# Kernel tuning notes

Measured on AMD Instinct MI355X. Metric: run time of the kernel, lower is better.

## Reference

```python
import jax, jax.numpy as jnp
import numpy as np

# dims: S spaces, B batch, T tokens, D = dense_dim = concept_dim, K codebook size
S, B, T, D, K = 8, 8, 2048, 64, 512
BN_EPS = 1e-3  # keras BatchNormalization default


def setup_inputs() -> dict:
    key = jax.random.key(0)
    k0, k1, k2 = jax.random.split(key, 3)
    x = jax.random.normal(k0, (B, T, D), jnp.float32)
    W = jax.random.normal(k1, (S, D, D), jnp.float32) * 0.1   # per-space Dense kernels
    b = jnp.zeros((S, D), jnp.float32)                         # per-space Dense biases
    gamma = jnp.ones((S, D), jnp.float32)                      # BN scale
    beta = jnp.zeros((S, D), jnp.float32)                      # BN shift
    bn_mean = jnp.zeros((S, D), jnp.float32)                   # BN moving mean
    bn_var = jnp.ones((S, D), jnp.float32)                     # BN moving var
    E = jax.random.normal(k2, (S, K, D), jnp.float32)          # per-space codebooks
    return dict(x=x, W=W, b=b, gamma=gamma, beta=beta,
                bn_mean=bn_mean, bn_var=bn_var, E=E)


def reference(x, W, b, gamma, beta, bn_mean, bn_var, E):
    # per-space projection: Dense -> BatchNorm (inference) -> softmax gate
    proj = jnp.einsum('btd,sde->sbte', x, W) + b[:, None, None, :]          # [S,B,T,D]
    inv = jax.lax.rsqrt(bn_var + BN_EPS)
    bn = gamma[:, None, None, :] * (proj - bn_mean[:, None, None, :]) * inv[:, None, None, :] \
         + beta[:, None, None, :]
    att = jax.nn.softmax(bn, axis=-1)
    z = x[None] * att                                                       # z_e_att, [S,B,T,D]

    # squared euclidean distance to each code; argmin(norm) == argmin(dist^2)
    d2 = (jnp.sum(z * z, axis=-1, keepdims=True)
          - 2.0 * jnp.einsum('sbtc,skc->sbtk', z, E)
          + jnp.sum(E * E, axis=-1)[:, None, None, :])                      # [S,B,T,K]
    z_k = jnp.argmin(d2, axis=-1)                                           # [S,B,T] int

    # gather nearest codes per space, then add_n over spaces (set_att != 0)
    z_q_s = E[jnp.arange(S)[:, None, None], z_k]                            # [S,B,T,D]
    z_q = jnp.sum(z_q_s, axis=0)                                            # [B,T,D]
    z_e = jnp.sum(z, axis=0)                                                # [B,T,D]
    z_k = z_k.astype(jnp.int64) if z_k.dtype != jnp.int64 else z_k          # tf.argmin -> int64
    return z_q, z_e, z_k
```

## Files before the change

### kernel.cpp

```cpp
#include <hip/hip_runtime.h>
#include <cfloat>
#include <cmath>

#define SN 8
#define DN 64
#define KN 512
#define NN 16384
#define CK 64
#define REPAIR_THR 2e-3f
#define GAP_IK 4u
#define MAXFLAG 32768

#define WS_CNT 0
#define WS_SCL 16
#define WS_OFF (16 + SN*DN)
#define WS_E2  (WS_OFF + SN*DN)
#define WS_ENT (WS_E2 + SN*KN)
#define WS_WTH (WS_ENT + MAXFLAG)
#define WS_WTL (WS_WTH + SN*64*32)
#define WS_EH  (WS_WTL + SN*64*32)
#define WS_EL  (WS_EH + SN*KN*32)
#define WS_ZP  (WS_EL + SN*KN*32)
#define WS_E2S (WS_ZP + SN*NN*DN)
#define WS_END (WS_E2S + SN*KN)

#define LDS_ZH 0
#define LDS_ZL 16384
#define LDS_E0 32768
#define LDS_TOTAL 65536

#define FB_LDS_R2    17408
#define FB_LDS_TAIL  33792
#define FB_LDS_TOTAL 34816

typedef __attribute__((ext_vector_type(8))) short bf16x8;
typedef __attribute__((ext_vector_type(4))) short s16x4;
typedef __attribute__((ext_vector_type(4))) float f32x4;

__device__ inline short bf_hi(float f, float& rem) {
    unsigned u = __float_as_uint(f);
    unsigned r = (u + 0x7fffu + ((u >> 16) & 1u)) & 0xffff0000u;
    rem = f - __uint_as_float(r);
    return (short)(r >> 16);
}
__device__ inline short bf_rn(float f) {
    unsigned u = __float_as_uint(f);
    return (short)((u + 0x7fffu + ((u >> 16) & 1u)) >> 16);
}
__device__ inline void cvt4(float a, float b, float c, float d, s16x4& h, s16x4& l) {
    float r0, r1, r2, r3;
    h.x = bf_hi(a, r0); h.y = bf_hi(b, r1); h.z = bf_hi(c, r2); h.w = bf_hi(d, r3);
    l.x = bf_rn(r0); l.y = bf_rn(r1); l.z = bf_rn(r2); l.w = bf_rn(r3);
}
__device__ inline float bf2f(unsigned short h) {
    return __uint_as_float(((unsigned)h) << 16);
}

union U8 { bf16x8 v; s16x4 q[2]; };

__global__ void prep_all_kernel(const float* __restrict__ b, const float* __restrict__ gamma,
                                const float* __restrict__ beta, const float* __restrict__ bmean,
                                const float* __restrict__ bvar, const float* __restrict__ W,
                                const float* __restrict__ E, float* __restrict__ ws) {
    __shared__ float wt[64][65];
    const int blk = blockIdx.x, tid = threadIdx.x;
    if (blk < 256) {
        int idx = blk * 256 + tid;
        int sk = idx >> 4, c4 = idx & 15;
        int k = sk & (KN - 1);
        float4 g = ((const float4*)E)[(size_t)sk * 16 + c4];
        s16x4 h4, l4;
        cvt4(g.x, g.y, g.z, g.w, h4, l4);
        size_t off = ((size_t)sk * 128 + c4 * 8) ^ ((k & 7) << 4);
        *(s16x4*)((char*)(ws + WS_EH) + off) = h4;
        *(s16x4*)((char*)(ws + WS_EL) + off) = l4;
    } else if (blk < 264) {
        int s = blk - 256;
        #pragma unroll
        for (int r = 0; r < 4; ++r) {
            int i = r * 256 + tid;
            float4 g = ((const float4*)W)[(size_t)s * 1024 + i];
            int d = i >> 4, c4 = i & 15;
            wt[d][c4 * 4 + 0] = g.x; wt[d][c4 * 4 + 1] = g.y;
            wt[d][c4 * 4 + 2] = g.z; wt[d][c4 * 4 + 3] = g.w;
        }
        __syncthreads();
        #pragma unroll
        for (int r = 0; r < 4; ++r) {
            int j = r * 256 + tid;
            int e = j >> 4, c4 = j & 15;
            s16x4 h4, l4;
            cvt4(wt[c4 * 4 + 0][e], wt[c4 * 4 + 1][e], wt[c4 * 4 + 2][e], wt[c4 * 4 + 3][e], h4, l4);
            size_t off = (size_t)(s * 64 + e) * 128 + c4 * 8;
            *(s16x4*)((char*)(ws + WS_WTH) + off) = h4;
            *(s16x4*)((char*)(ws + WS_WTL) + off) = l4;
        }
    } else {
        if (blk == 264 && tid < 16) ((int*)ws)[tid] = 0;
        int t2 = (blk - 264) * 256 + tid;
        if (t2 < SN * KN) {
            const float* er = E + (size_t)t2 * DN;
            double a = 0.0;
            for (int d = 0; d < DN; ++d) { double v = (double)er[d]; a = fma(v, v, a); }
            ws[WS_E2 + t2]  = (float)a;
            ws[WS_E2S + t2] = (float)(a * 4096.0);
        }
        int u = t2 - SN * KN;
        if (u >= 0 && u < SN * DN) {
            double inv = 1.0 / sqrt((double)bvar[u] + 0.001);
            double sc  = (double)gamma[u] * inv;
            ws[WS_SCL + u] = (float)sc;
            ws[WS_OFF + u] = (float)(((double)b[u] - (double)bmean[u]) * sc + (double)beta[u]);
        }
    }
}

__global__ void prep_kernel(const float* __restrict__ b, const float* __restrict__ gamma,
                            const float* __restrict__ beta, const float* __restrict__ bmean,
                            const float* __restrict__ bvar, const float* __restrict__ E,
                            float* __restrict__ ws) {
    int tid = blockIdx.x * 256 + threadIdx.x;
    if (tid < SN * KN) {
        const float* er = E + (size_t)tid * DN;
        double a = 0.0;
        for (int d = 0; d < DN; ++d) { double v = (double)er[d]; a = fma(v, v, a); }
        ws[WS_E2 + tid] = (float)a;
    }
    int u = tid - SN * KN;
    if (u >= 0 && u < SN * DN) {
        double inv = 1.0 / sqrt((double)bvar[u] + 0.001);
        double sc  = (double)gamma[u] * inv;
        ws[WS_SCL + u] = (float)sc;
        ws[WS_OFF + u] = (float)(((double)b[u] - (double)bmean[u]) * sc + (double)beta[u]);
    }
}

__launch_bounds__(512, 4)
__global__ void main_kernel(const float* __restrict__ x, float* __restrict__ ws,
                            float* __restrict__ out, int entcap) {
    extern __shared__ char smraw[];
    const int tid = threadIdx.x;
    const int s  = blockIdx.y;
    const int n0 = blockIdx.x * 128;
    const int lane = tid & 63;
    const int w    = tid >> 6;
    const int cc   = lane & 15;
    const int kq   = lane >> 4;
    const int arow = w * 16 + cc;
    const int axor = (arow & 7) << 4;

    const char* eimg_h = (const char*)(ws + WS_EH) + (size_t)s * KN * 128;
    const char* eimg_l = (const char*)(ws + WS_EL) + (size_t)s * KN * 128;

    float4 pf0 = *(const float4*)(eimg_h + tid * 16);
    float4 pf1 = *(const float4*)(eimg_l + tid * 16);

    U8 xah[2], xal[2];
    #pragma unroll
    for (int ks = 0; ks < 2; ++ks) {
        const float* xr = x + (size_t)(n0 + arow) * DN + ks * 32 + kq * 8;
        float4 a = *(const float4*)xr;
        float4 b2 = *(const float4*)(xr + 4);
        s16x4 h0, l0, h1, l1;
        cvt4(a.x, a.y, a.z, a.w, h0, l0);
        cvt4(b2.x, b2.y, b2.z, b2.w, h1, l1);
        xah[ks].q[0] = h0; xah[ks].q[1] = h1;
        xal[ks].q[0] = l0; xal[ks].q[1] = l1;
    }

    const char* wimg_h = (const char*)(ws + WS_WTH) + (size_t)s * 64 * 128;
    const char* wimg_l = (const char*)(ws + WS_WTL) + (size_t)s * 64 * 128;
    f32x4 pa[4];
    #pragma unroll
    for (int nt = 0; nt < 4; ++nt) pa[nt] = (f32x4){0.f, 0.f, 0.f, 0.f};
    #pragma unroll
    for (int ks = 0; ks < 2; ++ks) {
        #pragma unroll
        for (int nt = 0; nt < 4; ++nt) {
            int brow = nt * 16 + cc;
            bf16x8 bh = *(const bf16x8*)(wimg_h + brow * 128 + ks * 64 + kq * 16);
            bf16x8 bl = *(const bf16x8*)(wimg_l + brow * 128 + ks * 64 + kq * 16);
            pa[nt] = __builtin_amdgcn_mfma_f32_16x16x32_bf16(xah[ks].v, bh, pa[nt], 0, 0, 0);
            pa[nt] = __builtin_amdgcn_mfma_f32_16x16x32_bf16(xah[ks].v, bl, pa[nt], 0, 0, 0);
            pa[nt] = __builtin_amdgcn_mfma_f32_16x16x32_bf16(xal[ks].v, bh, pa[nt], 0, 0, 0);
        }
    }

    float sclv[4], oflv[4];
    #pragma unroll
    for (int nt = 0; nt < 4; ++nt) {
        sclv[nt] = ws[WS_SCL + s * 64 + nt * 16 + cc];
        oflv[nt] = ws[WS_OFF + s * 64 + nt * 16 + cc];
    }
    float zzq[4];
    #pragma unroll
    for (int r = 0; r < 4; ++r) {
        int t = w * 16 + kq * 4 + r;
        float v0 = fmaf(pa[0][r], sclv[0], oflv[0]);
        float v1 = fmaf(pa[1][r], sclv[1], oflv[1]);
        float v2 = fmaf(pa[2][r], sclv[2], oflv[2]);
        float v3 = fmaf(pa[3][r], sclv[3], oflv[3]);
        float mx = fmaxf(fmaxf(v0, v1), fmaxf(v2, v3));
        mx = fmaxf(mx, __shfl_xor(mx, 1)); mx = fmaxf(mx, __shfl_xor(mx, 2));
        mx = fmaxf(mx, __shfl_xor(mx, 4)); mx = fmaxf(mx, __shfl_xor(mx, 8));
        float e0 = __expf(v0 - mx), e1 = __expf(v1 - mx);
        float e2v = __expf(v2 - mx), e3 = __expf(v3 - mx);
        float sm = e0 + e1 + e2v + e3;
        sm += __shfl_xor(sm, 1); sm += __shfl_xor(sm, 2);
        sm += __shfl_xor(sm, 4); sm += __shfl_xor(sm, 8);
        float inv = 1.0f / sm;
        float att[4] = { e0 * inv, e1 * inv, e2v * inv, e3 * inv };
        float zz = 0.f;
        int txor = (t & 7) << 4;
        #pragma unroll
        for (int nt = 0; nt < 4; ++nt) {
            int e = nt * 16 + cc;
            float xv = x[(size_t)(n0 + t) * DN + e];
            float z = xv * att[nt];
            zz += z * z;
            float rem; short zh = bf_hi(z, rem); short zl = bf_rn(rem);
            int zoff = (t * 128 + e * 2) ^ txor;
            *(short*)(smraw + LDS_ZH + zoff) = zh;
            *(short*)(smraw + LDS_ZL + zoff) = zl;
        }
        zz += __shfl_xor(zz, 1); zz += __shfl_xor(zz, 2);
        zz += __shfl_xor(zz, 4); zz += __shfl_xor(zz, 8);
        zzq[r] = (zz + 16.f) * 4096.f;
    }

    bf16x8 zah[2], zal[2];
    #pragma unroll
    for (int ks = 0; ks < 2; ++ks) {
        int aoff = (arow * 128 + kq * 16 + ks * 64) ^ axor;
        zah[ks] = *(const bf16x8*)(smraw + LDS_ZH + aoff);
        zal[ks] = *(const bf16x8*)(smraw + LDS_ZL + aoff);
    }

    {
        char* eb = smraw + LDS_E0;
        *(float4*)(eb + tid * 16) = pf0;
        *(float4*)(eb + 8192 + tid * 16) = pf1;
    }
    __syncthreads();

    #pragma unroll
    for (int j = 0; j < 4; ++j) {
        int a = tid + j * 512;
        int t = a >> 4, q = a & 15;
        int off = (t * 128 + q * 8) ^ ((t & 7) << 4);
        s16x4 h = *(const s16x4*)(smraw + LDS_ZH + off);
        s16x4 l = *(const s16x4*)(smraw + LDS_ZL + off);
        float4 zv;
        zv.x = bf2f((unsigned short)h.x) + bf2f((unsigned short)l.x);
        zv.y = bf2f((unsigned short)h.y) + bf2f((unsigned short)l.y);
        zv.z = bf2f((unsigned short)h.z) + bf2f((unsigned short)l.z);
        zv.w = bf2f((unsigned short)h.w) + bf2f((unsigned short)l.w);
        ((float4*)(ws + WS_ZP))[((size_t)s * NN + n0 + t) * 16 + q] = zv;
    }

    unsigned m1[4], m2[4];
    #pragma unroll
    for (int r = 0; r < 4; ++r) { m1[r] = 0xFFFFFFFFu; m2[r] = 0xFFFFFFFFu; }

    int p = 0;
    #pragma unroll 1
    for (int c = 0; c < KN / CK; ++c) {
        const char* ebuf = smraw + LDS_E0 + p * 16384;
        int kk = c * CK;
        if (c < KN / CK - 1) {
            pf0 = *(const float4*)(eimg_h + (size_t)(kk + CK) * 128 + tid * 16);
            pf1 = *(const float4*)(eimg_l + (size_t)(kk + CK) * 128 + tid * 16);
        }
        float e2v[4];
        #pragma unroll
        for (int nt = 0; nt < 4; ++nt) e2v[nt] = ws[WS_E2S + s * KN + kk + nt * 16 + cc];

        f32x4 acc[4];
        #pragma unroll
        for (int nt = 0; nt < 4; ++nt) acc[nt] = (f32x4){0.f, 0.f, 0.f, 0.f};
        #pragma unroll
        for (int ks = 0; ks < 2; ++ks) {
            #pragma unroll
            for (int nt = 0; nt < 4; ++nt) {
                int brow = nt * 16 + cc;
                int boff = (brow * 128 + kq * 16 + ks * 64) ^ ((brow & 7) << 4);
                bf16x8 bh = *(const bf16x8*)(ebuf + boff);
                bf16x8 bl = *(const bf16x8*)(ebuf + 8192 + boff);
                acc[nt] = __builtin_amdgcn_mfma_f32_16x16x32_bf16(zah[ks], bh, acc[nt], 0, 0, 0);
                acc[nt] = __builtin_amdgcn_mfma_f32_16x16x32_bf16(zah[ks], bl, acc[nt], 0, 0, 0);
                acc[nt] = __builtin_amdgcn_mfma_f32_16x16x32_bf16(zal[ks], bh, acc[nt], 0, 0, 0);
            }
        }
        #pragma unroll
        for (int nt = 0; nt < 4; ++nt) {
            unsigned kx = (unsigned)(kk + nt * 16 + cc);
            #pragma unroll
            for (int r = 0; r < 4; ++r) {
                float cell = fmaf(-8192.f, acc[nt][r], zzq[r] + e2v[nt]);
                unsigned key = (((unsigned)cell) << 9) | kx;
                m2[r] = min(m2[r], max(m1[r], key));
                m1[r] = min(m1[r], key);
            }
        }
        if (c < KN / CK - 1) {
            char* nb = smraw + LDS_E0 + (p ^ 1) * 16384;
            *(float4*)(nb + tid * 16) = pf0;
            *(float4*)(nb + 8192 + tid * 16) = pf1;
            __syncthreads();
            p ^= 1;
        }
    }

    #pragma unroll
    for (int mask = 1; mask <= 8; mask <<= 1) {
        #pragma unroll
        for (int r = 0; r < 4; ++r) {
            unsigned o1 = (unsigned)__shfl_xor((int)m1[r], mask);
            unsigned o2 = (unsigned)__shfl_xor((int)m2[r], mask);
            unsigned hi = max(m1[r], o1);
            m1[r] = min(m1[r], o1);
            m2[r] = min(min(m2[r], o2), hi);
        }
    }
    #pragma unroll
    for (int r = 0; r < 4; ++r) {
        int n = n0 + w * 16 + kq * 4 + r;
        if (cc == 0) {
            int k1 = (int)(m1[r] & 511u);
            out[2 * NN * DN + s * NN + n] = (float)k1;
            if ((m2[r] >> 9) - (m1[r] >> 9) <= GAP_IK) {
                int idx = atomicAdd((int*)ws, 1);
                if (idx < entcap) ((int*)ws)[WS_ENT + idx] = (s << 14) | n;
            }
        }
    }
}

__launch_bounds__(256, 4)
__global__ void main_fb_kernel(const float* __restrict__ x, const float* __restrict__ W,
                               const float* __restrict__ E, float* __restrict__ ws,
                               float* __restrict__ out, int entcap) {
    extern __shared__ char smraw[];
    float4* xs4 = (float4*)smraw;
    float4* ws4 = (float4*)(smraw + FB_LDS_R2);
    char* ehb = smraw;
    char* elb = smraw + 8192;
    char* zhb = smraw + FB_LDS_R2;
    char* zlb = smraw + FB_LDS_R2 + 8192;
    float* tailf = (float*)(smraw + FB_LDS_TAIL);
    float* e2s = tailf; float* scl = tailf + 64; float* ofl = tailf + 128; float* zzs = tailf + 192;

    const int tid = threadIdx.x;
    const int tg = tid >> 4, lg = tid & 15;
    const int s  = blockIdx.y;
    const int n0 = blockIdx.x * 64;
    const float4* xg4 = (const float4*)x;
    const float4* Wg4 = (const float4*)W;
    const float4* Eg4 = (const float4*)E;

    #pragma unroll
    for (int r = 0; r < 4; ++r) {
        int i = r * 256 + tid;
        xs4[(i >> 4) * 17 + (i & 15)] = xg4[n0 * 16 + i];
        ws4[i] = Wg4[s * 1024 + i];
    }
    if (tid < 64) { scl[tid] = ws[WS_SCL + s * 64 + tid]; ofl[tid] = ws[WS_OFF + s * 64 + tid]; }
    __syncthreads();

    float pa[4][4];
    #pragma unroll
    for (int ti = 0; ti < 4; ++ti)
        #pragma unroll
        for (int j = 0; j < 4; ++j) pa[ti][j] = 0.f;
    #pragma unroll 4
    for (int c = 0; c < 16; ++c) {
        float4 xv[4], wv[4];
        #pragma unroll
        for (int ti = 0; ti < 4; ++ti) xv[ti] = xs4[(tg * 4 + ti) * 17 + c];
        #pragma unroll
        for (int dd = 0; dd < 4; ++dd) wv[dd] = ws4[(c * 4 + dd) * 16 + lg];
        #pragma unroll
        for (int ti = 0; ti < 4; ++ti) {
            float a0 = pa[ti][0], a1 = pa[ti][1], a2 = pa[ti][2], a3 = pa[ti][3];
            a0 = fmaf(xv[ti].x, wv[0].x, a0); a0 = fmaf(xv[ti].y, wv[1].x, a0);
            a0 = fmaf(xv[ti].z, wv[2].x, a0); a0 = fmaf(xv[ti].w, wv[3].x, a0);
            a1 = fmaf(xv[ti].x, wv[0].y, a1); a1 = fmaf(xv[ti].y, wv[1].y, a1);
            a1 = fmaf(xv[ti].z, wv[2].y, a1); a1 = fmaf(xv[ti].w, wv[3].y, a1);
            a2 = fmaf(xv[ti].x, wv[0].z, a2); a2 = fmaf(xv[ti].y, wv[1].z, a2);
            a2 = fmaf(xv[ti].z, wv[2].z, a2); a2 = fmaf(xv[ti].w, wv[3].z, a2);
            a3 = fmaf(xv[ti].x, wv[0].w, a3); a3 = fmaf(xv[ti].y, wv[1].w, a3);
            a3 = fmaf(xv[ti].z, wv[2].w, a3); a3 = fmaf(xv[ti].w, wv[3].w, a3);
            pa[ti][0] = a0; pa[ti][1] = a1; pa[ti][2] = a2; pa[ti][3] = a3;
        }
    }
    __syncthreads();

    {
        float s0 = scl[lg * 4 + 0], s1 = scl[lg * 4 + 1], s2 = scl[lg * 4 + 2], s3 = scl[lg * 4 + 3];
        float o0 = ofl[lg * 4 + 0], o1 = ofl[lg * 4 + 1], o2 = ofl[lg * 4 + 2], o3 = ofl[lg * 4 + 3];
        #pragma unroll
        for (int ti = 0; ti < 4; ++ti) {
            int t = tg * 4 + ti;
            float v0 = fmaf(pa[ti][0], s0, o0);
            float v1 = fmaf(pa[ti][1], s1, o1);
            float v2 = fmaf(pa[ti][2], s2, o2);
            float v3 = fmaf(pa[ti][3], s3, o3);
            float mx = fmaxf(fmaxf(v0, v1), fmaxf(v2, v3));
            mx = fmaxf(mx, __shfl_xor(mx, 1)); mx = fmaxf(mx, __shfl_xor(mx, 2));
            mx = fmaxf(mx, __shfl_xor(mx, 4)); mx = fmaxf(mx, __shfl_xor(mx, 8));
            float e0 = expf(v0 - mx), e1 = expf(v1 - mx), e2v = expf(v2 - mx), e3 = expf(v3 - mx);
            float sm = e0 + e1 + e2v + e3;
            sm += __shfl_xor(sm, 1); sm += __shfl_xor(sm, 2);
            sm += __shfl_xor(sm, 4); sm += __shfl_xor(sm, 8);
            float inv = 1.0f / sm;
            float4 xv = xs4[t * 17 + lg];
            float z0 = xv.x * (e0 * inv), z1 = xv.y * (e1 * inv);
            float z2 = xv.z * (e2v * inv), z3 = xv.w * (e3 * inv);
            float zz = z0 * z0 + z1 * z1 + z2 * z2 + z3 * z3;
            zz += __shfl_xor(zz, 1); zz += __shfl_xor(zz, 2);
            zz += __shfl_xor(zz, 4); zz += __shfl_xor(zz, 8);
            if (lg == 0) zzs[t] = zz;
            s16x4 h4, l4;
            cvt4(z0, z1, z2, z3, h4, l4);
            int zoff = (t * 128 + lg * 8) ^ ((t & 7) << 4);
            *(s16x4*)(zhb + zoff) = h4;
            *(s16x4*)(zlb + zoff) = l4;
            float* pz = out + NN * DN + (size_t)(n0 + t) * DN + lg * 4;
            atomicAdd(pz + 0, z0); atomicAdd(pz + 1, z1);
            atomicAdd(pz + 2, z2); atomicAdd(pz + 3, z3);
        }
    }
    __syncthreads();

    const int lane = tid & 63;
    const int w    = tid >> 6;
    const int arow = w * 16 + (lane & 15);
    const int kg16 = (lane >> 4) * 16;
    const int axor = (arow & 7) << 4;
    const int abase = arow * 128 + kg16;

    float zzv[4];
    #pragma unroll
    for (int r = 0; r < 4; ++r) zzv[r] = zzs[w * 16 + (lane >> 4) * 4 + r];

    float m1[4], m2[4]; int k1[4];
    #pragma unroll
    for (int r = 0; r < 4; ++r) { m1[r] = FLT_MAX; m2[r] = FLT_MAX; k1[r] = 0x7fffffff; }

    for (int kk = 0; kk < KN; kk += CK) {
        __syncthreads();
        #pragma unroll
        for (int r = 0; r < 4; ++r) {
            int i = r * 256 + tid;
            float4 g = Eg4[(s * KN + kk) * 16 + i];
            int row = i >> 4, c4 = i & 15;
            s16x4 h4, l4;
            cvt4(g.x, g.y, g.z, g.w, h4, l4);
            int off = (row * 128 + c4 * 8) ^ ((row & 7) << 4);
            *(s16x4*)(ehb + off) = h4;
            *(s16x4*)(elb + off) = l4;
        }
        if (tid < 64) e2s[tid] = ws[WS_E2 + s * KN + kk + tid];
        __syncthreads();

        f32x4 acc[4];
        #pragma unroll
        for (int nt = 0; nt < 4; ++nt) acc[nt] = (f32x4){0.f, 0.f, 0.f, 0.f};
        #pragma unroll
        for (int ks = 0; ks < 2; ++ks) {
            int aoff = (abase + ks * 64) ^ axor;
            bf16x8 ah = *(const bf16x8*)(zhb + aoff);
            bf16x8 al = *(const bf16x8*)(zlb + aoff);
            #pragma unroll
            for (int nt = 0; nt < 4; ++nt) {
                int brow = nt * 16 + (lane & 15);
                int boff = (brow * 128 + kg16 + ks * 64) ^ ((brow & 7) << 4);
                bf16x8 bh = *(const bf16x8*)(ehb + boff);
                bf16x8 bl = *(const bf16x8*)(elb + boff);
                acc[nt] = __builtin_amdgcn_mfma_f32_16x16x32_bf16(ah, bh, acc[nt], 0, 0, 0);
                acc[nt] = __builtin_amdgcn_mfma_f32_16x16x32_bf16(ah, bl, acc[nt], 0, 0, 0);
                acc[nt] = __builtin_amdgcn_mfma_f32_16x16x32_bf16(al, bh, acc[nt], 0, 0, 0);
            }
        }
        #pragma unroll
        for (int nt = 0; nt < 4; ++nt) {
            float e2v = e2s[nt * 16 + (lane & 15)];
            int kx = kk + nt * 16 + (lane & 15);
            #pragma unroll
            for (int r = 0; r < 4; ++r) {
                float d2 = fmaf(-2.0f, acc[nt][r], zzv[r]) + e2v;
                if (d2 < m1[r]) { m2[r] = m1[r]; m1[r] = d2; k1[r] = kx; }
                else if (d2 < m2[r]) { m2[r] = d2; }
            }
        }
    }

    #pragma unroll
    for (int mask = 1; mask <= 8; mask <<= 1) {
        #pragma unroll
        for (int r = 0; r < 4; ++r) {
            float om1 = __shfl_xor(m1[r], mask);
            int   ok1 = __shfl_xor(k1[r], mask);
            float om2 = __shfl_xor(m2[r], mask);
            bool better = (om1 < m1[r]) || (om1 == m1[r] && ok1 < k1[r]);
            float nm2 = better ? fminf(m1[r], om2) : fminf(om1, m2[r]);
            if (better) { m1[r] = om1; k1[r] = ok1; }
            m2[r] = nm2;
        }
    }
    #pragma unroll
    for (int r = 0; r < 4; ++r) {
        int t = w * 16 + (lane >> 4) * 4 + r;
        int n = n0 + t;
        if ((lane & 15) == 0) {
            out[2 * NN * DN + s * NN + n] = (float)k1[r];
            if (m2[r] - m1[r] < REPAIR_THR) {
                int idx = atomicAdd((int*)ws, 1);
                if (idx < entcap) ((int*)ws)[WS_ENT + idx] = (s << 14) | n;
            }
        }
        int kb = __shfl(k1[r], lane & 48);
        float4 eg = Eg4[(s * KN + kb) * 16 + (lane & 15)];
        float* q = out + (size_t)n * DN + (lane & 15) * 4;
        atomicAdd(q + 0, eg.x); atomicAdd(q + 1, eg.y);
        atomicAdd(q + 2, eg.z); atomicAdd(q + 3, eg.w);
    }
}

__global__ void reduce_kernel(const float* __restrict__ E, const float* __restrict__ ws,
                              float* __restrict__ out) {
    int idx = blockIdx.x * 256 + threadIdx.x;
    int n = idx >> 4, c = idx & 15;
    const float4* zp4 = (const float4*)(ws + WS_ZP);
    float4 ze = make_float4(0.f, 0.f, 0.f, 0.f);
    #pragma unroll
    for (int s = 0; s < SN; ++s) {
        float4 v = zp4[((size_t)s * NN + n) * 16 + c];
        ze.x += v.x; ze.y += v.y; ze.z += v.z; ze.w += v.w;
    }
    ((float4*)out)[NN * 16 + (size_t)n * 16 + c] = ze;

    float4 zq = make_float4(0.f, 0.f, 0.f, 0.f);
    #pragma unroll
    for (int s = 0; s < SN; ++s) {
        int k = (int)(out[2 * NN * DN + s * NN + n] + 0.5f);
        float4 e = ((const float4*)E)[((size_t)s * KN + k) * 16 + c];
        zq.x += e.x; zq.y += e.y; zq.z += e.z; zq.w += e.w;
    }
    ((float4*)out)[(size_t)n * 16 + c] = zq;
}

__global__ void repair_kernel(const float* __restrict__ x, const float* __restrict__ W,
                              const float* __restrict__ b, const float* __restrict__ gamma,
                              const float* __restrict__ beta, const float* __restrict__ bmean,
                              const float* __restrict__ bvar, const float* __restrict__ E,
                              float* __restrict__ ws, float* __restrict__ out, int entcap) {
    __shared__ double zd[64];
    __shared__ double red[256];
    __shared__ int redk[256];
    __shared__ double zzsh;
    __shared__ int shk[2];
    int cnt = ((int*)ws)[0]; if (cnt > entcap) cnt = entcap;
    const int tid = threadIdx.x;
    for (int idx = blockIdx.x; idx < cnt; idx += gridDim.x) {
        int code = ((int*)ws)[WS_ENT + idx];
        int s = code >> 14, n = code & (NN - 1);
        int e = tid & 63, q = tid >> 6;
        const float* xrow = x + (size_t)n * 64;
        double p0 = 0.0, p1 = 0.0, p2 = 0.0, p3 = 0.0;
        for (int d = q * 16; d < q * 16 + 16; d += 4) {
            p0 = fma((double)xrow[d],     (double)W[((size_t)s * 64 + d) * 64 + e],     p0);
            p1 = fma((double)xrow[d + 1], (double)W[((size_t)s * 64 + d + 1) * 64 + e], p1);
            p2 = fma((double)xrow[d + 2], (double)W[((size_t)s * 64 + d + 2) * 64 + e], p2);
            p3 = fma((double)xrow[d + 3], (double)W[((size_t)s * 64 + d + 3) * 64 + e], p3);
        }
        red[tid] = (p0 + p1) + (p2 + p3);
        __syncthreads();
        if (tid < 64) {
            double proj = (red[tid] + red[tid + 64]) + (red[tid + 128] + red[tid + 192]);
            double inv = 1.0 / sqrt((double)bvar[s * 64 + e] + 0.001);
            double bn = (double)gamma[s * 64 + e] * ((proj + (double)b[s * 64 + e]) - (double)bmean[s * 64 + e]) * inv
                      + (double)beta[s * 64 + e];
            double m = bn;
            #pragma unroll
            for (int mask = 1; mask <= 32; mask <<= 1) m = fmax(m, __shfl_xor(m, mask));
            double ex = exp(bn - m);
            double sm = ex;
            #pragma unroll
            for (int mask = 1; mask <= 32; mask <<= 1) sm += __shfl_xor(sm, mask);
            double z = (double)xrow[e] * (ex / sm);
            zd[e] = z;
            double zz = z * z;
            #pragma unroll
            for (int mask = 1; mask <= 32; mask <<= 1) zz += __shfl_xor(zz, mask);
            if (tid == 0) zzsh = zz;
        }
        __syncthreads();
        double bv = DBL_MAX; int bk = 1 << 30;
        for (int k = tid; k < KN; k += 256) {
            const float* er = E + ((size_t)s * KN + k) * 64;
            double d0 = 0.0, d1 = 0.0, d2a = 0.0, d3 = 0.0;
            double f0 = 0.0, f1 = 0.0, f2 = 0.0, f3 = 0.0;
            for (int d = 0; d < 64; d += 4) {
                double e0 = (double)er[d], e1 = (double)er[d + 1];
                double e2d = (double)er[d + 2], e3d = (double)er[d + 3];
                d0 = fma(zd[d], e0, d0);     d1 = fma(zd[d + 1], e1, d1);
                d2a = fma(zd[d + 2], e2d, d2a); d3 = fma(zd[d + 3], e3d, d3);
                f0 = fma(e0, e0, f0); f1 = fma(e1, e1, f1);
                f2 = fma(e2d, e2d, f2); f3 = fma(e3d, e3d, f3);
            }
            double dot = (d0 + d1) + (d2a + d3);
            double e2t = (f0 + f1) + (f2 + f3);
            double d2v = (zzsh - 2.0 * dot) + e2t;
            if (d2v < bv) { bv = d2v; bk = k; }
        }
        #pragma unroll
        for (int mask = 1; mask <= 32; mask <<= 1) {
            double ov = __shfl_xor(bv, mask);
            int   ok = __shfl_xor(bk, mask);
            if (ov < bv || (ov == bv && ok < bk)) { bv = ov; bk = ok; }
        }
        if ((tid & 63) == 0) { red[tid >> 6] = bv; redk[tid >> 6] = bk; }
        __syncthreads();
        if (tid == 0) {
            double m = red[0]; int mk = redk[0];
            for (int i = 1; i < 4; ++i)
                if (red[i] < m || (red[i] == m && redk[i] < mk)) { m = red[i]; mk = redk[i]; }
            int kold = (int)(out[2 * NN * 64 + s * NN + n] + 0.5f);
            shk[0] = mk; shk[1] = kold;
            out[2 * NN * 64 + s * NN + n] = (float)mk;
        }
        __syncthreads();
        int mk = shk[0], kold = shk[1];
        if (mk != kold && tid < 64)
            atomicAdd(out + n * 64 + tid, E[((size_t)s * KN + mk) * 64 + tid] - E[((size_t)s * KN + kold) * 64 + tid]);
        __syncthreads();
    }
}

extern "C" void kernel_launch(void* const* d_in, const int* in_sizes, int n_in,
                              void* d_out, int out_size, void* d_ws, size_t ws_size,
                              hipStream_t stream) {
    const float* x     = (const float*)d_in[0];
    const float* W     = (const float*)d_in[1];
    const float* b     = (const float*)d_in[2];
    const float* gamma = (const float*)d_in[3];
    const float* beta  = (const float*)d_in[4];
    const float* bmean = (const float*)d_in[5];
    const float* bvar  = (const float*)d_in[6];
    const float* E     = (const float*)d_in[7];
    float* out = (float*)d_out;
    float* ws  = (float*)d_ws;

    bool staged = ws_size >= (size_t)WS_END * 4;

    long avail = (long)(ws_size / 4) - WS_ENT - 16;
    if (avail < 0) avail = 0;
    int entcap = (int)(avail > MAXFLAG ? MAXFLAG : avail);
    if (staged) entcap = MAXFLAG;

    if (staged) {
        hipFuncSetAttribute((const void*)main_kernel, hipFuncAttributeMaxDynamicSharedMemorySize, LDS_TOTAL);
        prep_all_kernel<<<282, 256, 0, stream>>>(b, gamma, beta, bmean, bvar, W, E, ws);
        dim3 grid(128, 8);
        main_kernel<<<grid, 512, LDS_TOTAL, stream>>>(x, ws, out, entcap);
        reduce_kernel<<<1024, 256, 0, stream>>>(E, ws, out);
    } else {
        hipMemsetAsync(d_ws, 0, 64, stream);
        prep_kernel<<<18, 256, 0, stream>>>(b, gamma, beta, bmean, bvar, E, ws);
        hipMemsetAsync(d_out, 0, (size_t)(2 * NN * DN) * sizeof(float), stream);
        dim3 grid(256, 8);
        main_fb_kernel<<<grid, 256, FB_LDS_TOTAL, stream>>>(x, W, E, ws, out, entcap);
    }
    repair_kernel<<<2048, 256, 0, stream>>>(x, W, b, gamma, beta, bmean, bvar, E, ws, out, entcap);
}
```

Before: 150.3 us.

## Read codebook MFMA operands directly from global memory instead of LDS double buffer

Removes the double-buffered LDS staging of the bf16 hi/lo codebook images in the main distance kernel, so each wave loads B operands straight from global or L2 memory. Only the z tiles stay in shared memory, so the allocation halves and launch bounds are raised to allow more resident blocks. The prep kernel stops writing the XOR-swizzled layout to match. This drops the per-chunk barriers and LDS stores, but every wave now re-reads the same codebook rows from cache with no prefetch, which may expose memory latency.

```diff
diff --git a/kernel.cpp b/kernel.cpp
--- a/kernel.cpp
+++ b/kernel.cpp
@@ -26,8 +26,7 @@
 
 #define LDS_ZH 0
 #define LDS_ZL 16384
-#define LDS_E0 32768
-#define LDS_TOTAL 65536
+#define LDS_TOTAL 32768
 
 #define FB_LDS_R2    17408
 #define FB_LDS_TAIL  33792
@@ -67,11 +66,10 @@
     if (blk < 256) {
         int idx = blk * 256 + tid;
         int sk = idx >> 4, c4 = idx & 15;
-        int k = sk & (KN - 1);
         float4 g = ((const float4*)E)[(size_t)sk * 16 + c4];
         s16x4 h4, l4;
         cvt4(g.x, g.y, g.z, g.w, h4, l4);
-        size_t off = ((size_t)sk * 128 + c4 * 8) ^ ((k & 7) << 4);
+        size_t off = (size_t)sk * 128 + c4 * 8;
         *(s16x4*)((char*)(ws + WS_EH) + off) = h4;
         *(s16x4*)((char*)(ws + WS_EL) + off) = l4;
     } else if (blk < 264) {
@@ -135,7 +133,7 @@
     }
 }
 
-__launch_bounds__(512, 4)
+__launch_bounds__(512, 8)
 __global__ void main_kernel(const float* __restrict__ x, float* __restrict__ ws,
                             float* __restrict__ out, int entcap) {
     extern __shared__ char smraw[];
@@ -151,9 +149,6 @@
 
     const char* eimg_h = (const char*)(ws + WS_EH) + (size_t)s * KN * 128;
     const char* eimg_l = (const char*)(ws + WS_EL) + (size_t)s * KN * 128;
-
-    float4 pf0 = *(const float4*)(eimg_h + tid * 16);
-    float4 pf1 = *(const float4*)(eimg_l + tid * 16);
 
     U8 xah[2], xal[2];
     #pragma unroll
@@ -235,12 +230,6 @@
         zah[ks] = *(const bf16x8*)(smraw + LDS_ZH + aoff);
         zal[ks] = *(const bf16x8*)(smraw + LDS_ZL + aoff);
     }
-
-    {
-        char* eb = smraw + LDS_E0;
-        *(float4*)(eb + tid * 16) = pf0;
-        *(float4*)(eb + 8192 + tid * 16) = pf1;
-    }
     __syncthreads();
 
     #pragma unroll
@@ -262,15 +251,9 @@
     #pragma unroll
     for (int r = 0; r < 4; ++r) { m1[r] = 0xFFFFFFFFu; m2[r] = 0xFFFFFFFFu; }
 
-    int p = 0;
     #pragma unroll 1
     for (int c = 0; c < KN / CK; ++c) {
-        const char* ebuf = smraw + LDS_E0 + p * 16384;
         int kk = c * CK;
-        if (c < KN / CK - 1) {
-            pf0 = *(const float4*)(eimg_h + (size_t)(kk + CK) * 128 + tid * 16);
-            pf1 = *(const float4*)(eimg_l + (size_t)(kk + CK) * 128 + tid * 16);
-        }
         float e2v[4];
         #pragma unroll
         for (int nt = 0; nt < 4; ++nt) e2v[nt] = ws[WS_E2S + s * KN + kk + nt * 16 + cc];
@@ -282,10 +265,9 @@
         for (int ks = 0; ks < 2; ++ks) {
             #pragma unroll
             for (int nt = 0; nt < 4; ++nt) {
-                int brow = nt * 16 + cc;
-                int boff = (brow * 128 + kq * 16 + ks * 64) ^ ((brow & 7) << 4);
-                bf16x8 bh = *(const bf16x8*)(ebuf + boff);
-                bf16x8 bl = *(const bf16x8*)(ebuf + 8192 + boff);
+                size_t boff = (size_t)(kk + nt * 16 + cc) * 128 + ks * 64 + kq * 16;
+                bf16x8 bh = *(const bf16x8*)(eimg_h + boff);
+                bf16x8 bl = *(const bf16x8*)(eimg_l + boff);
                 acc[nt] = __builtin_amdgcn_mfma_f32_16x16x32_bf16(zah[ks], bh, acc[nt], 0, 0, 0);
                 acc[nt] = __builtin_amdgcn_mfma_f32_16x16x32_bf16(zah[ks], bl, acc[nt], 0, 0, 0);
                 acc[nt] = __builtin_amdgcn_mfma_f32_16x16x32_bf16(zal[ks], bh, acc[nt], 0, 0, 0);
@@ -301,13 +283,6 @@
                 m2[r] = min(m2[r], max(m1[r], key));
                 m1[r] = min(m1[r], key);
             }
-        }
-        if (c < KN / CK - 1) {
-            char* nb = smraw + LDS_E0 + (p ^ 1) * 16384;
-            *(float4*)(nb + tid * 16) = pf0;
-            *(float4*)(nb + 8192 + tid * 16) = pf1;
-            __syncthreads();
-            p ^= 1;
         }
     }
 
@@ -660,7 +635,6 @@
     if (staged) entcap = MAXFLAG;
 
     if (staged) {
-        hipFuncSetAttribute((const void*)main_kernel, hipFuncAttributeMaxDynamicSharedMemorySize, LDS_TOTAL);
         prep_all_kernel<<<282, 256, 0, stream>>>(b, gamma, beta, bmean, bvar, W, E, ws);
         dim3 grid(128, 8);
         main_kernel<<<grid, 512, LDS_TOTAL, stream>>>(x, ws, out, entcap);
```

Result: slower. 267.6 us (+78.0%).
